# Performance work log

Measured on AMD Instinct MI355X. Metric: run time of the kernel, lower is better.

The kernel has to match this reference:

```python
import jax, jax.numpy as jnp
import numpy as np

D_MODEL = 768
N_HEADS = 12
HEAD_DIM = D_MODEL // N_HEADS


def setup_inputs() -> dict:
    key = jax.random.key(0)
    ks = jax.random.split(key, 12)
    B, S, D = 2, 2048, D_MODEL
    inp = {
        "query": jax.random.normal(ks[0], (B, S, D), jnp.float32),
        "key": jax.random.normal(ks[1], (B, S, D), jnp.float32),
        "value": jax.random.normal(ks[2], (B, S, D), jnp.float32),
        "attention_mask": jax.random.randint(ks[3], (B, 1, 1, S), 0, 2, jnp.int32),
        # Linear params (torch convention: y = x @ W.T + b)
        "wq": jax.random.normal(ks[4], (D, D), jnp.float32) * (1.0 / np.sqrt(D)),
        "bq": jnp.zeros((D,), jnp.float32),
        "wk": jax.random.normal(ks[5], (D, D), jnp.float32) * (1.0 / np.sqrt(D)),
        "bk": jnp.zeros((D,), jnp.float32),
        "wv": jax.random.normal(ks[6], (D, D), jnp.float32) * (1.0 / np.sqrt(D)),
        "bv": jnp.zeros((D,), jnp.float32),
        "wo": jax.random.normal(ks[7], (D, D), jnp.float32) * (1.0 / np.sqrt(D)),
        "bo": jnp.zeros((D,), jnp.float32),
    }
    return inp


def reference(query, key, value, attention_mask, wq, bq, wk, bk, wv, bv, wo, bo):
    B, S, D = query.shape
    H, Dh = N_HEADS, HEAD_DIM
    q = (query @ wq.T + bq).reshape(B, S, H, Dh)
    k = (key @ wk.T + bk).reshape(B, S, H, Dh)
    v = (value @ wv.T + bv).reshape(B, S, H, Dh)
    scale = 1.0 / np.sqrt(Dh).astype(np.float32)
    # scores: [B, H, S, S]
    scores = jnp.einsum("bqhd,bkhd->bhqk", q, k) * scale
    scores = jnp.where(attention_mask == 0, jnp.float32(-1e9), scores)
    probs = jax.nn.softmax(scores, axis=-1)  # dropout_rate=0.0 -> identity
    out = jnp.einsum("bhqk,bkhd->bqhd", probs, v).reshape(B, S, D)
    out = out @ wo.T + bo
    return out, probs
```

## Files before the change

### kernel.cpp

```cpp
#include <hip/hip_runtime.h>
#include <math.h>

#define NB 2
#define NS 2048
#define ND 768
#define NH 12
#define DH 64

#define BM 128
#define BN 128
#define BK 64

typedef __attribute__((ext_vector_type(8))) short short8;
typedef __attribute__((ext_vector_type(8))) __bf16 bf16x8;
typedef __attribute__((ext_vector_type(4))) float f32x4;

static __device__ inline unsigned short f2bf(float f) {
    unsigned int u = __float_as_uint(f);
    unsigned int r = (u + 0x7FFFu + ((u >> 16) & 1u)) >> 16;
    return (unsigned short)r;
}

static __device__ inline bf16x8 ld_bf8(const unsigned short* p) {
    short8 s = *(const short8*)p;
    return __builtin_bit_cast(bf16x8, s);
}

static __device__ inline void gload_lds16(const void* g, void* l) {
    __builtin_amdgcn_global_load_lds(
        (const __attribute__((address_space(1))) void*)g,
        (__attribute__((address_space(3))) void*)l, 16, 0, 0);
}

struct CvtArgs {
    const float* src[7];
    unsigned short* dst[7];
    int n8[7];
};

__global__ __launch_bounds__(256) void cvt_kernel(CvtArgs a) {
    const int t = blockIdx.y;
    const float* __restrict__ s = a.src[t];
    unsigned short* __restrict__ d = a.dst[t];
    const int n8 = a.n8[t];
    for (int i = blockIdx.x * 256 + threadIdx.x; i < n8; i += gridDim.x * 256) {
        float4 f0 = ((const float4*)s)[(size_t)i * 2];
        float4 f1 = ((const float4*)s)[(size_t)i * 2 + 1];
        unsigned short pk[8] = { f2bf(f0.x), f2bf(f0.y), f2bf(f0.z), f2bf(f0.w),
                                 f2bf(f1.x), f2bf(f1.y), f2bf(f1.z), f2bf(f1.w) };
        *(short8*)(d + (size_t)i * 8) = *(short8*)pk;
    }
}

template<int MODE>
__global__ __launch_bounds__(256) void gemm_kernel(
    const unsigned short* __restrict__ A0, const unsigned short* __restrict__ A1,
    const unsigned short* __restrict__ A2,
    const unsigned short* __restrict__ B0, const unsigned short* __restrict__ B1,
    const unsigned short* __restrict__ B2,
    const float* __restrict__ bias0, const float* __restrict__ bias1,
    const float* __restrict__ bias2,
    void* __restrict__ out0, void* __restrict__ out1, void* __restrict__ out2)
{
    const int p = blockIdx.z;
    const unsigned short* A = (p == 0) ? A0 : (p == 1) ? A1 : A2;
    const unsigned short* B = (p == 0) ? B0 : (p == 1) ? B1 : B2;
    const float* bias = (p == 0) ? bias0 : (p == 1) ? bias1 : bias2;
    void* outp = (p == 0) ? out0 : (p == 1) ? out1 : out2;
    const float qscale = (MODE == 0 && p == 0) ? 0.125f : 1.0f;

    const int m0 = blockIdx.y * BM;
    const int n0 = blockIdx.x * BN;
    const int tid = threadIdx.x;
    const int wave = tid >> 6, lane = tid & 63;
    const int wr = wave >> 1, wc = wave & 1;
    const int c = lane & 15, quad = lane >> 4;

    __shared__ __align__(16) unsigned short As[BM * BK];
    __shared__ __align__(16) unsigned short Bs[BN * BK];

    f32x4 acc[4][4] = {};

    const int srow0 = wave * 8 + (lane >> 3);
    const int slane8 = lane & 7;

    for (int k0 = 0; k0 < ND; k0 += BK) {
#pragma unroll
        for (int j = 0; j < 4; ++j) {
            const int row = j * 32 + srow0;
            const int chunk = slane8 ^ (row & 7);
            gload_lds16(A + (size_t)(m0 + row) * ND + k0 + chunk * 8,
                        &As[j * 2048 + wave * 512]);
            gload_lds16(B + (size_t)(n0 + row) * ND + k0 + chunk * 8,
                        &Bs[j * 2048 + wave * 512]);
        }
        __syncthreads();

#pragma unroll
        for (int ks = 0; ks < 2; ++ks) {
            bf16x8 af[4], bfv[4];
#pragma unroll
            for (int i = 0; i < 4; ++i) {
                const int rA = wr * 64 + i * 16 + c;
                af[i] = ld_bf8(&As[rA * 64 + ((ks * 32 + quad * 8) ^ ((rA & 7) << 3))]);
                const int rB = wc * 64 + i * 16 + c;
                bfv[i] = ld_bf8(&Bs[rB * 64 + ((ks * 32 + quad * 8) ^ ((rB & 7) << 3))]);
            }
#pragma unroll
            for (int i = 0; i < 4; ++i)
#pragma unroll
                for (int j = 0; j < 4; ++j)
                    acc[i][j] = __builtin_amdgcn_mfma_f32_16x16x32_bf16(
                        af[i], bfv[j], acc[i][j], 0, 0, 0);
        }
        __syncthreads();
    }

    float bj[4];
#pragma unroll
    for (int j = 0; j < 4; ++j) bj[j] = bias[n0 + wc * 64 + j * 16 + c];

    if (MODE == 0) {
        unsigned short* out = (unsigned short*)outp;
        const int h = (n0 >> 6) + wc;
#pragma unroll
        for (int i = 0; i < 4; ++i) {
#pragma unroll
            for (int r = 0; r < 4; ++r) {
                const int m = m0 + wr * 64 + i * 16 + quad * 4 + r;
                const int bb = m >> 11, s = m & (NS - 1);
                unsigned short* orow = out + (((size_t)bb * NH + h) * NS + s) * DH;
#pragma unroll
                for (int j = 0; j < 4; ++j)
                    orow[j * 16 + c] = f2bf((acc[i][j][r] + bj[j]) * qscale);
            }
        }
    } else {
        float* out = (float*)outp;
#pragma unroll
        for (int i = 0; i < 4; ++i) {
#pragma unroll
            for (int r = 0; r < 4; ++r) {
                const int m = m0 + wr * 64 + i * 16 + quad * 4 + r;
                float* orow = out + (size_t)m * ND + n0 + wc * 64;
#pragma unroll
                for (int j = 0; j < 4; ++j)
                    orow[j * 16 + c] = acc[i][j][r] + bj[j];
            }
        }
    }
}

__global__ __launch_bounds__(256) void attn_kernel(
    const unsigned short* __restrict__ qg, const unsigned short* __restrict__ kg,
    const unsigned short* __restrict__ vg, const int* __restrict__ mask,
    float* __restrict__ probs, unsigned short* __restrict__ attnout)
{
    const int bh = blockIdx.y;
    const int b = bh / NH, h = bh % NH;
    const int q0 = blockIdx.x * 64;
    const int tid  = threadIdx.x;
    const int w    = tid >> 6;
    const int lane = tid & 63;
    const int quad = lane >> 4;
    const int c    = lane & 15;

    __shared__ union {
        unsigned short Ka[2][128 * 64];
        struct {
            unsigned short Ks[2][64 * 64];
            unsigned short Vt[2][64][72];
            unsigned short Ps[4][16][72];
        } b;
    } sm;
    __shared__ float madd[NS];

    const int* mrow = mask + b * NS;
    for (int i = tid; i < NS; i += 256) madd[i] = mrow[i] ? 0.0f : -1.0e9f;

    const size_t hb = (size_t)bh * NS;

    const unsigned short* qrow = qg + (hb + q0 + w * 16 + c) * DH;
    bf16x8 afrag0 = ld_bf8(qrow + quad * 8);
    bf16x8 afrag1 = ld_bf8(qrow + 32 + quad * 8);

    const int srow0 = w * 8 + (lane >> 3);
    const int schunk = (lane & 7) ^ (lane >> 3);
    const int rsw = (quad ^ (c & 7)) << 3;

    float l_r[4] = {0.f, 0.f, 0.f, 0.f};

#pragma unroll
    for (int j = 0; j < 4; ++j) {
        const int row = j * 32 + srow0;
        gload_lds16(kg + (hb + row) * DH + schunk * 8,
                    &sm.Ka[0][(j * 32 + w * 8) * 64]);
    }
    __syncthreads();

    int cur = 0;
    for (int kt = 0; kt < NS / 128; ++kt) {
        const int k0 = kt * 128;
        if (kt + 1 < NS / 128) {
            const int k0n = k0 + 128;
#pragma unroll
            for (int j = 0; j < 4; ++j) {
                const int row = j * 32 + srow0;
                gload_lds16(kg + (hb + k0n + row) * DH + schunk * 8,
                            &sm.Ka[cur ^ 1][(j * 32 + w * 8) * 64]);
            }
        }
        const unsigned short* Kc = &sm.Ka[cur][0];
#pragma unroll
        for (int nt = 0; nt < 8; ++nt) {
            const int row = nt * 16 + c;
            bf16x8 b0 = ld_bf8(&Kc[row * 64 + rsw]);
            bf16x8 b1 = ld_bf8(&Kc[row * 64 + (rsw ^ 32)]);
            f32x4 C = {0.f, 0.f, 0.f, 0.f};
            C = __builtin_amdgcn_mfma_f32_16x16x32_bf16(afrag0, b0, C, 0, 0, 0);
            C = __builtin_amdgcn_mfma_f32_16x16x32_bf16(afrag1, b1, C, 0, 0, 0);
            const float ma = madd[k0 + nt * 16 + c];
#pragma unroll
            for (int r = 0; r < 4; ++r) l_r[r] += __expf(C[r] + ma);
        }
        __syncthreads();
        cur ^= 1;
    }

    float linv[4];
#pragma unroll
    for (int r = 0; r < 4; ++r) {
        float s = l_r[r];
        s += __shfl_xor(s, 1);
        s += __shfl_xor(s, 2);
        s += __shfl_xor(s, 4);
        s += __shfl_xor(s, 8);
        linv[r] = 1.0f / s;
    }

    f32x4 o[4] = {{0.f,0.f,0.f,0.f},{0.f,0.f,0.f,0.f},{0.f,0.f,0.f,0.f},{0.f,0.f,0.f,0.f}};
    const size_t prow = ((size_t)bh * NS + q0 + w * 16) * NS;
    const int d0 = w * 16;

    short8 vx0, vx1;
#pragma unroll
    for (int j = 0; j < 2; ++j) {
        const int row = j * 32 + srow0;
        gload_lds16(kg + (hb + row) * DH + schunk * 8,
                    &sm.b.Ks[0][(j * 32 + w * 8) * 64]);
    }
    {
        const unsigned short* vsrc = vg + (hb + lane) * DH + d0;
        vx0 = *(const short8*)vsrc;
        vx1 = *(const short8*)(vsrc + 8);
    }
#pragma unroll
    for (int j = 0; j < 8; ++j) {
        sm.b.Vt[0][d0 + j][lane]     = (unsigned short)vx0[j];
        sm.b.Vt[0][d0 + 8 + j][lane] = (unsigned short)vx1[j];
    }
    __syncthreads();

    cur = 0;
    for (int kt = 0; kt < NS / 64; ++kt) {
        const int k0 = kt * 64;
        const bool more = (kt + 1 < NS / 64);
        if (more) {
            const int k0n = k0 + 64;
#pragma unroll
            for (int j = 0; j < 2; ++j) {
                const int row = j * 32 + srow0;
                gload_lds16(kg + (hb + k0n + row) * DH + schunk * 8,
                            &sm.b.Ks[cur ^ 1][(j * 32 + w * 8) * 64]);
            }
            const unsigned short* vsrc = vg + (hb + k0n + lane) * DH + d0;
            vx0 = *(const short8*)vsrc;
            vx1 = *(const short8*)(vsrc + 8);
        }

        const unsigned short* Kc = &sm.b.Ks[cur][0];
#pragma unroll
        for (int nt = 0; nt < 4; ++nt) {
            const int row = nt * 16 + c;
            bf16x8 b0 = ld_bf8(&Kc[row * 64 + rsw]);
            bf16x8 b1 = ld_bf8(&Kc[row * 64 + (rsw ^ 32)]);
            f32x4 C = {0.f, 0.f, 0.f, 0.f};
            C = __builtin_amdgcn_mfma_f32_16x16x32_bf16(afrag0, b0, C, 0, 0, 0);
            C = __builtin_amdgcn_mfma_f32_16x16x32_bf16(afrag1, b1, C, 0, 0, 0);
            const float ma = madd[k0 + nt * 16 + c];
#pragma unroll
            for (int r = 0; r < 4; ++r) {
                float pv = __expf(C[r] + ma) * linv[r];
                probs[prow + (size_t)(quad * 4 + r) * NS + k0 + nt * 16 + c] = pv;
                sm.b.Ps[w][quad * 4 + r][nt * 16 + c] = f2bf(pv);
            }
        }

        bf16x8 pa0 = ld_bf8(&sm.b.Ps[w][c][quad * 8]);
        bf16x8 pa1 = ld_bf8(&sm.b.Ps[w][c][32 + quad * 8]);
        __builtin_amdgcn_s_setprio(1);
#pragma unroll
        for (int dt = 0; dt < 4; ++dt) {
            bf16x8 vb0 = ld_bf8(&sm.b.Vt[cur][dt * 16 + c][quad * 8]);
            bf16x8 vb1 = ld_bf8(&sm.b.Vt[cur][dt * 16 + c][32 + quad * 8]);
            o[dt] = __builtin_amdgcn_mfma_f32_16x16x32_bf16(pa0, vb0, o[dt], 0, 0, 0);
            o[dt] = __builtin_amdgcn_mfma_f32_16x16x32_bf16(pa1, vb1, o[dt], 0, 0, 0);
        }
        __builtin_amdgcn_s_setprio(0);

        if (more) {
#pragma unroll
            for (int j = 0; j < 8; ++j) {
                sm.b.Vt[cur ^ 1][d0 + j][lane]     = (unsigned short)vx0[j];
                sm.b.Vt[cur ^ 1][d0 + 8 + j][lane] = (unsigned short)vx1[j];
            }
        }
        __syncthreads();
        cur ^= 1;
    }

#pragma unroll
    for (int dt = 0; dt < 4; ++dt) {
#pragma unroll
        for (int r = 0; r < 4; ++r) {
            int s = q0 + w * 16 + quad * 4 + r;
            attnout[((size_t)b * NS + s) * ND + h * DH + dt * 16 + c] = f2bf(o[dt][r]);
        }
    }
}

extern "C" void kernel_launch(void* const* d_in, const int* in_sizes, int n_in,
                              void* d_out, int out_size, void* d_ws, size_t ws_size,
                              hipStream_t stream) {
    const float* query = (const float*)d_in[0];
    const float* key   = (const float*)d_in[1];
    const float* value = (const float*)d_in[2];
    const int*   amask = (const int*)d_in[3];
    const float* wq = (const float*)d_in[4];
    const float* bq = (const float*)d_in[5];
    const float* wk = (const float*)d_in[6];
    const float* bk = (const float*)d_in[7];
    const float* wv = (const float*)d_in[8];
    const float* bv = (const float*)d_in[9];
    const float* wo = (const float*)d_in[10];
    const float* bo = (const float*)d_in[11];

    const size_t elems  = (size_t)NB * NS * ND;
    const size_t welems = (size_t)ND * ND;

    float* out   = (float*)d_out;
    float* probs = out + elems;

    unsigned short* xq_bf = (unsigned short*)probs;
    unsigned short* xk_bf = xq_bf + elems;
    unsigned short* xv_bf = xk_bf + elems;

    unsigned short* qbf   = (unsigned short*)d_ws;
    unsigned short* kbf   = qbf + elems;
    unsigned short* vbf   = kbf + elems;
    unsigned short* abf   = vbf + elems;
    unsigned short* wq_bf = abf + elems;
    unsigned short* wk_bf = wq_bf + welems;
    unsigned short* wv_bf = wk_bf + welems;
    unsigned short* wo_bf = wv_bf + welems;

    CvtArgs ca;
    ca.src[0] = query; ca.dst[0] = xq_bf; ca.n8[0] = (int)(elems / 8);
    ca.src[1] = key;   ca.dst[1] = xk_bf; ca.n8[1] = (int)(elems / 8);
    ca.src[2] = value; ca.dst[2] = xv_bf; ca.n8[2] = (int)(elems / 8);
    ca.src[3] = wq;    ca.dst[3] = wq_bf; ca.n8[3] = (int)(welems / 8);
    ca.src[4] = wk;    ca.dst[4] = wk_bf; ca.n8[4] = (int)(welems / 8);
    ca.src[5] = wv;    ca.dst[5] = wv_bf; ca.n8[5] = (int)(welems / 8);
    ca.src[6] = wo;    ca.dst[6] = wo_bf; ca.n8[6] = (int)(welems / 8);
    cvt_kernel<<<dim3(512, 7, 1), 256, 0, stream>>>(ca);

    gemm_kernel<0><<<dim3(ND / BN, (NB * NS) / BM, 3), 256, 0, stream>>>(
        xq_bf, xk_bf, xv_bf, wq_bf, wk_bf, wv_bf, bq, bk, bv, qbf, kbf, vbf);

    attn_kernel<<<dim3(NS / 64, NB * NH), 256, 0, stream>>>(
        qbf, kbf, vbf, amask, probs, abf);

    gemm_kernel<1><<<dim3(ND / BN, (NB * NS) / BM, 1), 256, 0, stream>>>(
        abf, abf, abf, wo_bf, wo_bf, wo_bf, bo, bo, bo, out, out, out);
}
```

Before: 617.8 us.

## Deepen attention K/V prefetch with counted vmcnt barriers and XCD-aware block mapping

Restructures both passes of the attention kernel so that loads run two tiles ahead. Raw s_barrier plus explicit vmcnt/lgkmcnt waits replace __syncthreads, so in-flight global-to-LDS loads are not drained at every iteration. Blocks are remapped so each XCD handles a contiguous set of (batch, head) pairs, which should improve L2 reuse of K/V. It also drops the setprio hints and peels the last iteration; the hand-counted vmcnt values risk correctness if the compiler emits a different number of memory ops.

Result: faster. 576.5 us (-6.7%).

```diff
diff --git a/kernel.cpp b/kernel.cpp
--- a/kernel.cpp
+++ b/kernel.cpp
@@ -31,6 +31,19 @@
         (const __attribute__((address_space(1))) void*)g,
         (__attribute__((address_space(3))) void*)l, 16, 0, 0);
 }
+
+#define BAR_VM4()  do { asm volatile("s_waitcnt vmcnt(4) lgkmcnt(0)" ::: "memory"); \
+                        __builtin_amdgcn_sched_barrier(0); \
+                        __builtin_amdgcn_s_barrier(); \
+                        __builtin_amdgcn_sched_barrier(0); } while (0)
+#define BAR_VM0()  do { asm volatile("s_waitcnt vmcnt(0) lgkmcnt(0)" ::: "memory"); \
+                        __builtin_amdgcn_sched_barrier(0); \
+                        __builtin_amdgcn_s_barrier(); \
+                        __builtin_amdgcn_sched_barrier(0); } while (0)
+#define BAR_LGKM() do { asm volatile("s_waitcnt lgkmcnt(0)" ::: "memory"); \
+                        __builtin_amdgcn_sched_barrier(0); \
+                        __builtin_amdgcn_s_barrier(); \
+                        __builtin_amdgcn_sched_barrier(0); } while (0)
 
 struct CvtArgs {
     const float* src[7];
@@ -156,9 +169,13 @@
     const unsigned short* __restrict__ vg, const int* __restrict__ mask,
     float* __restrict__ probs, unsigned short* __restrict__ attnout)
 {
-    const int bh = blockIdx.y;
+    const int lin = blockIdx.x + blockIdx.y * gridDim.x;
+    const int xcd = lin & 7;
+    const int jj  = lin >> 3;
+    const int bh  = xcd * 3 + (jj >> 5);
+    const int q0  = (jj & 31) * 64;
+
     const int b = bh / NH, h = bh % NH;
-    const int q0 = blockIdx.x * 64;
     const int tid  = threadIdx.x;
     const int w    = tid >> 6;
     const int lane = tid & 63;
@@ -189,27 +206,26 @@
     const int rsw = (quad ^ (c & 7)) << 3;
 
     float l_r[4] = {0.f, 0.f, 0.f, 0.f};
+    const int NTA = NS / 128;
 
 #pragma unroll
     for (int j = 0; j < 4; ++j) {
         const int row = j * 32 + srow0;
-        gload_lds16(kg + (hb + row) * DH + schunk * 8,
+        gload_lds16(kg + (hb + 0 + row) * DH + schunk * 8,
                     &sm.Ka[0][(j * 32 + w * 8) * 64]);
     }
-    __syncthreads();
-
-    int cur = 0;
-    for (int kt = 0; kt < NS / 128; ++kt) {
+#pragma unroll
+    for (int j = 0; j < 4; ++j) {
+        const int row = j * 32 + srow0;
+        gload_lds16(kg + (hb + 128 + row) * DH + schunk * 8,
+                    &sm.Ka[1][(j * 32 + w * 8) * 64]);
+    }
+
+    for (int kt = 0; kt < NTA - 1; ++kt) {
+        const int cur = kt & 1;
+        BAR_VM4();
+
         const int k0 = kt * 128;
-        if (kt + 1 < NS / 128) {
-            const int k0n = k0 + 128;
-#pragma unroll
-            for (int j = 0; j < 4; ++j) {
-                const int row = j * 32 + srow0;
-                gload_lds16(kg + (hb + k0n + row) * DH + schunk * 8,
-                            &sm.Ka[cur ^ 1][(j * 32 + w * 8) * 64]);
-            }
-        }
         const unsigned short* Kc = &sm.Ka[cur][0];
 #pragma unroll
         for (int nt = 0; nt < 8; ++nt) {
@@ -223,8 +239,35 @@
 #pragma unroll
             for (int r = 0; r < 4; ++r) l_r[r] += __expf(C[r] + ma);
         }
-        __syncthreads();
-        cur ^= 1;
+
+        BAR_LGKM();
+        if (kt + 2 < NTA) {
+            const int k0n = (kt + 2) * 128;
+#pragma unroll
+            for (int j = 0; j < 4; ++j) {
+                const int row = j * 32 + srow0;
+                gload_lds16(kg + (hb + k0n + row) * DH + schunk * 8,
+                            &sm.Ka[cur][(j * 32 + w * 8) * 64]);
+            }
+        }
+    }
+    {
+        BAR_VM0();
+        const int kt = NTA - 1, cur = kt & 1;
+        const int k0 = kt * 128;
+        const unsigned short* Kc = &sm.Ka[cur][0];
+#pragma unroll
+        for (int nt = 0; nt < 8; ++nt) {
+            const int row = nt * 16 + c;
+            bf16x8 b0 = ld_bf8(&Kc[row * 64 + rsw]);
+            bf16x8 b1 = ld_bf8(&Kc[row * 64 + (rsw ^ 32)]);
+            f32x4 C = {0.f, 0.f, 0.f, 0.f};
+            C = __builtin_amdgcn_mfma_f32_16x16x32_bf16(afrag0, b0, C, 0, 0, 0);
+            C = __builtin_amdgcn_mfma_f32_16x16x32_bf16(afrag1, b1, C, 0, 0, 0);
+            const float ma = madd[k0 + nt * 16 + c];
+#pragma unroll
+            for (int r = 0; r < 4; ++r) l_r[r] += __expf(C[r] + ma);
+        }
     }
 
     float linv[4];
@@ -238,19 +281,23 @@
         linv[r] = 1.0f / s;
     }
 
+    __syncthreads();
+
     f32x4 o[4] = {{0.f,0.f,0.f,0.f},{0.f,0.f,0.f,0.f},{0.f,0.f,0.f,0.f},{0.f,0.f,0.f,0.f}};
     const size_t prow = ((size_t)bh * NS + q0 + w * 16) * NS;
     const int d0 = w * 16;
+    const int NTB = NS / 64;
 
     short8 vx0, vx1;
+
 #pragma unroll
     for (int j = 0; j < 2; ++j) {
         const int row = j * 32 + srow0;
-        gload_lds16(kg + (hb + row) * DH + schunk * 8,
+        gload_lds16(kg + (hb + 0 + row) * DH + schunk * 8,
                     &sm.b.Ks[0][(j * 32 + w * 8) * 64]);
     }
     {
-        const unsigned short* vsrc = vg + (hb + lane) * DH + d0;
+        const unsigned short* vsrc = vg + (hb + 0 + lane) * DH + d0;
         vx0 = *(const short8*)vsrc;
         vx1 = *(const short8*)(vsrc + 8);
     }
@@ -259,24 +306,22 @@
         sm.b.Vt[0][d0 + j][lane]     = (unsigned short)vx0[j];
         sm.b.Vt[0][d0 + 8 + j][lane] = (unsigned short)vx1[j];
     }
-    __syncthreads();
-
-    cur = 0;
-    for (int kt = 0; kt < NS / 64; ++kt) {
+#pragma unroll
+    for (int j = 0; j < 2; ++j) {
+        const int row = j * 32 + srow0;
+        gload_lds16(kg + (hb + 64 + row) * DH + schunk * 8,
+                    &sm.b.Ks[1][(j * 32 + w * 8) * 64]);
+    }
+    {
+        const unsigned short* vsrc = vg + (hb + 64 + lane) * DH + d0;
+        vx0 = *(const short8*)vsrc;
+        vx1 = *(const short8*)(vsrc + 8);
+    }
+    BAR_LGKM();
+
+    for (int kt = 0; kt < NTB - 1; ++kt) {
+        const int cur = kt & 1;
         const int k0 = kt * 64;
-        const bool more = (kt + 1 < NS / 64);
-        if (more) {
-            const int k0n = k0 + 64;
-#pragma unroll
-            for (int j = 0; j < 2; ++j) {
-                const int row = j * 32 + srow0;
-                gload_lds16(kg + (hb + k0n + row) * DH + schunk * 8,
-                            &sm.b.Ks[cur ^ 1][(j * 32 + w * 8) * 64]);
-            }
-            const unsigned short* vsrc = vg + (hb + k0n + lane) * DH + d0;
-            vx0 = *(const short8*)vsrc;
-            vx1 = *(const short8*)(vsrc + 8);
-        }
 
         const unsigned short* Kc = &sm.b.Ks[cur][0];
 #pragma unroll
@@ -295,10 +340,8 @@
                 sm.b.Ps[w][quad * 4 + r][nt * 16 + c] = f2bf(pv);
             }
         }
-
         bf16x8 pa0 = ld_bf8(&sm.b.Ps[w][c][quad * 8]);
         bf16x8 pa1 = ld_bf8(&sm.b.Ps[w][c][32 + quad * 8]);
-        __builtin_amdgcn_s_setprio(1);
 #pragma unroll
         for (int dt = 0; dt < 4; ++dt) {
             bf16x8 vb0 = ld_bf8(&sm.b.Vt[cur][dt * 16 + c][quad * 8]);
@@ -306,17 +349,57 @@
             o[dt] = __builtin_amdgcn_mfma_f32_16x16x32_bf16(pa0, vb0, o[dt], 0, 0, 0);
             o[dt] = __builtin_amdgcn_mfma_f32_16x16x32_bf16(pa1, vb1, o[dt], 0, 0, 0);
         }
-        __builtin_amdgcn_s_setprio(0);
-
-        if (more) {
-#pragma unroll
-            for (int j = 0; j < 8; ++j) {
-                sm.b.Vt[cur ^ 1][d0 + j][lane]     = (unsigned short)vx0[j];
-                sm.b.Vt[cur ^ 1][d0 + 8 + j][lane] = (unsigned short)vx1[j];
-            }
-        }
-        __syncthreads();
-        cur ^= 1;
+
+        BAR_LGKM();
+
+#pragma unroll
+        for (int j = 0; j < 8; ++j) {
+            sm.b.Vt[cur ^ 1][d0 + j][lane]     = (unsigned short)vx0[j];
+            sm.b.Vt[cur ^ 1][d0 + 8 + j][lane] = (unsigned short)vx1[j];
+        }
+        if (kt + 2 < NTB) {
+            const int k0n = (kt + 2) * 64;
+#pragma unroll
+            for (int j = 0; j < 2; ++j) {
+                const int row = j * 32 + srow0;
+                gload_lds16(kg + (hb + k0n + row) * DH + schunk * 8,
+                            &sm.b.Ks[cur][(j * 32 + w * 8) * 64]);
+            }
+            const unsigned short* vsrc = vg + (hb + k0n + lane) * DH + d0;
+            vx0 = *(const short8*)vsrc;
+            vx1 = *(const short8*)(vsrc + 8);
+        }
+        BAR_VM4();
+    }
+    {
+        const int kt = NTB - 1, cur = kt & 1;
+        const int k0 = kt * 64;
+        const unsigned short* Kc = &sm.b.Ks[cur][0];
+#pragma unroll
+        for (int nt = 0; nt < 4; ++nt) {
+            const int row = nt * 16 + c;
+            bf16x8 b0 = ld_bf8(&Kc[row * 64 + rsw]);
+            bf16x8 b1 = ld_bf8(&Kc[row * 64 + (rsw ^ 32)]);
+            f32x4 C = {0.f, 0.f, 0.f, 0.f};
+            C = __builtin_amdgcn_mfma_f32_16x16x32_bf16(afrag0, b0, C, 0, 0, 0);
+            C = __builtin_amdgcn_mfma_f32_16x16x32_bf16(afrag1, b1, C, 0, 0, 0);
+            const float ma = madd[k0 + nt * 16 + c];
+#pragma unroll
+            for (int r = 0; r < 4; ++r) {
+                float pv = __expf(C[r] + ma) * linv[r];
+                probs[prow + (size_t)(quad * 4 + r) * NS + k0 + nt * 16 + c] = pv;
+                sm.b.Ps[w][quad * 4 + r][nt * 16 + c] = f2bf(pv);
+            }
+        }
+        bf16x8 pa0 = ld_bf8(&sm.b.Ps[w][c][quad * 8]);
+        bf16x8 pa1 = ld_bf8(&sm.b.Ps[w][c][32 + quad * 8]);
+#pragma unroll
+        for (int dt = 0; dt < 4; ++dt) {
+            bf16x8 vb0 = ld_bf8(&sm.b.Vt[cur][dt * 16 + c][quad * 8]);
+            bf16x8 vb1 = ld_bf8(&sm.b.Vt[cur][dt * 16 + c][32 + quad * 8]);
+            o[dt] = __builtin_amdgcn_mfma_f32_16x16x32_bf16(pa0, vb0, o[dt], 0, 0, 0);
+            o[dt] = __builtin_amdgcn_mfma_f32_16x16x32_bf16(pa1, vb1, o[dt], 0, 0, 0);
+        }
     }
 
 #pragma unroll
```
